# Kernel optimization log

Measured on AMD Instinct MI355X. Metric: run time of the kernel, lower is better.

Reference implementation:

```python
import jax, jax.numpy as jnp
import numpy as np

N_BAND = 5  # module hardcodes self.n = 5 -> keeps |i-j| <= N_BAND-1 = 4


def setup_inputs() -> dict:
    key = jax.random.key(0)
    ks = jax.random.split(key, 6)
    B, L, H = 4, 2048, 1024
    s = 1.0 / np.sqrt(H)
    return {
        "q": jax.random.normal(ks[0], (B, L, H), jnp.float32),
        "k": jax.random.normal(ks[1], (B, L, H), jnp.float32),
        "Wq": jax.random.normal(ks[2], (H, H), jnp.float32) * s,
        "bq": jax.random.normal(ks[3], (H,), jnp.float32) * s,
        "Wk": jax.random.normal(ks[4], (H, H), jnp.float32) * s,
        "bk": jax.random.normal(ks[5], (H,), jnp.float32) * s,
    }


def reference(q, k, Wq, bq, Wk, bk):
    b, l, e = q.shape
    # nn.Linear: y = x @ W^T + b
    qs = jnp.einsum("ble,he->blh", q, Wq) + bq
    ks = jnp.einsum("ble,he->blh", k, Wk) + bk
    # dense QK^T logits, [b, l, l]
    logits = jnp.einsum("blh,bmh->blm", qs, ks)
    # banded mask: the torch loop zeroes offsets 0..n-1 on both sides -> |i-j| <= n-1
    idx = jnp.arange(l)
    band = jnp.abs(idx[:, None] - idx[None, :]) <= (N_BAND - 1)  # [l, l]
    neg_inf = jnp.array(-jnp.inf, dtype=logits.dtype)
    logits = jnp.where(band[None, :, :], logits, neg_inf)
    # every row contains its diagonal, so softmax is well-defined
    return jax.nn.softmax(logits, axis=-1)
```

## Files before the change

kernel.cpp:

```cpp
#include <hip/hip_runtime.h>
#include <math.h>

#define LSEQ 2048
#define HDIM 1024
#define BATCH 4
#define ROWS (BATCH * LSEQ)
#define NBAND 9

typedef __attribute__((ext_vector_type(8))) short bf16x8;
typedef __attribute__((ext_vector_type(4))) float f32x4;
typedef __attribute__((ext_vector_type(8))) unsigned short u16x8;
typedef __attribute__((ext_vector_type(4))) unsigned uintx4;

#define AS3 __attribute__((address_space(3)))
#define AS1 __attribute__((address_space(1)))

__device__ __forceinline__ void gload16(const void* gp, void* lp) {
    __builtin_amdgcn_global_load_lds((AS1 const unsigned*)gp, (AS3 unsigned*)lp, 16, 0, 0);
}

__device__ __forceinline__ unsigned short f2bf(float x) {
    unsigned u = __float_as_uint(x);
    u += 0x7FFFu + ((u >> 16) & 1u);
    return (unsigned short)(u >> 16);
}
__device__ __forceinline__ float bf2f(unsigned short h) {
    return __uint_as_float(((unsigned)h) << 16);
}

__device__ __forceinline__ void split8(float4 a, float4 b, bf16x8& hi, bf16x8& lo) {
    float v[8] = {a.x, a.y, a.z, a.w, b.x, b.y, b.z, b.w};
#pragma unroll
    for (int j = 0; j < 8; j++) {
        unsigned short h = f2bf(v[j]);
        hi[j] = (short)h;
        lo[j] = (short)f2bf(v[j] - bf2f(h));
    }
}

__device__ __forceinline__ void unpack8(uintx4 w0, uintx4 w1, bf16x8& hi, bf16x8& lo) {
    union { bf16x8 v; uintx4 u; } H, L;
    H.u[0] = __builtin_amdgcn_perm(w0[1], w0[0], 0x05040100u);
    H.u[1] = __builtin_amdgcn_perm(w0[3], w0[2], 0x05040100u);
    H.u[2] = __builtin_amdgcn_perm(w1[1], w1[0], 0x05040100u);
    H.u[3] = __builtin_amdgcn_perm(w1[3], w1[2], 0x05040100u);
    L.u[0] = __builtin_amdgcn_perm(w0[1], w0[0], 0x07060302u);
    L.u[1] = __builtin_amdgcn_perm(w0[3], w0[2], 0x07060302u);
    L.u[2] = __builtin_amdgcn_perm(w1[1], w1[0], 0x07060302u);
    L.u[3] = __builtin_amdgcn_perm(w1[3], w1[2], 0x07060302u);
    hi = H.v; lo = L.v;
}

__global__ __launch_bounds__(256) void wpart_kernel(const float* __restrict__ Wk,
                                                    const float* __restrict__ bq,
                                                    float* __restrict__ wpart) {
    const int b = blockIdx.x;
    const int c0 = threadIdx.x * 4;
    float4 acc = {0.f, 0.f, 0.f, 0.f};
#pragma unroll
    for (int hh = 0; hh < 16; hh++) {
        const int h = b * 16 + hh;
        const float s = bq[h];
        float4 v = *reinterpret_cast<const float4*>(&Wk[(size_t)h * HDIM + c0]);
        acc.x += v.x * s; acc.y += v.y * s; acc.z += v.z * s; acc.w += v.w * s;
    }
    *reinterpret_cast<float4*>(&wpart[(size_t)b * HDIM + c0]) = acc;
}

__global__ __launch_bounds__(256) void wreduce(const float* __restrict__ wpart,
                                               float* __restrict__ w) {
    const int c = blockIdx.x * 256 + threadIdx.x;
    float s = 0.f;
#pragma unroll
    for (int b = 0; b < 64; b++) s += wpart[(size_t)b * HDIM + c];
    w[c] = s;
}

__global__ __launch_bounds__(256) void transpose_convert(const float* __restrict__ Wq,
                                                         const float* __restrict__ Wk,
                                                         unsigned short* __restrict__ qhi,
                                                         unsigned short* __restrict__ qlo,
                                                         unsigned short* __restrict__ khi,
                                                         unsigned short* __restrict__ klo) {
    __shared__ float tile[64][65];
    const int z = blockIdx.z;
    const float* src = z ? Wk : Wq;
    unsigned short* dh = z ? khi : qhi;
    unsigned short* dl = z ? klo : qlo;
    const int n0 = blockIdx.x * 64;
    const int h0 = blockIdx.y * 64;
    const int tid = threadIdx.x;

#pragma unroll
    for (int p = 0; p < 4; p++) {
        const int h = p * 16 + (tid >> 4);
        const int n = (tid & 15) * 4;
        float4 v = *reinterpret_cast<const float4*>(&src[(size_t)(h0 + h) * HDIM + n0 + n]);
        tile[h][n + 0] = v.x; tile[h][n + 1] = v.y; tile[h][n + 2] = v.z; tile[h][n + 3] = v.w;
    }
    __syncthreads();
#pragma unroll
    for (int p = 0; p < 2; p++) {
        const int n = p * 32 + (tid >> 3);
        const int h = (tid & 7) * 8;
        u16x8 hv, lv;
#pragma unroll
        for (int j = 0; j < 8; j++) {
            float x = tile[h + j][n];
            unsigned short hb = f2bf(x);
            hv[j] = hb;
            lv[j] = f2bf(x - bf2f(hb));
        }
        *reinterpret_cast<u16x8*>(&dh[(size_t)(n0 + n) * HDIM + h0 + h]) = hv;
        *reinterpret_cast<u16x8*>(&dl[(size_t)(n0 + n) * HDIM + h0 + h]) = lv;
    }
}

__global__ __launch_bounds__(256) void convert_k_beta(const float* __restrict__ k,
                                                      const float* __restrict__ w,
                                                      unsigned short* __restrict__ Xhi,
                                                      unsigned short* __restrict__ Xlo,
                                                      float* __restrict__ beta) {
    __shared__ float red[4];
    const int r = blockIdx.x;
    const int t = threadIdx.x;
    float4 v = *reinterpret_cast<const float4*>(&k[(size_t)r * HDIM + t * 4]);
    float4 wv = *reinterpret_cast<const float4*>(&w[t * 4]);
    ushort4 h, l;
    h.x = f2bf(v.x); l.x = f2bf(v.x - bf2f(h.x));
    h.y = f2bf(v.y); l.y = f2bf(v.y - bf2f(h.y));
    h.z = f2bf(v.z); l.z = f2bf(v.z - bf2f(h.z));
    h.w = f2bf(v.w); l.w = f2bf(v.w - bf2f(h.w));
    reinterpret_cast<ushort4*>(Xhi)[(size_t)r * 256 + t] = h;
    reinterpret_cast<ushort4*>(Xlo)[(size_t)r * 256 + t] = l;
    float d = v.x * wv.x + v.y * wv.y + v.z * wv.z + v.w * wv.w;
#pragma unroll
    for (int off = 32; off > 0; off >>= 1) d += __shfl_xor(d, off, 64);
    if ((t & 63) == 0) red[t >> 6] = d;
    __syncthreads();
    if (t == 0) beta[r] = red[0] + red[1] + red[2] + red[3];
}

__global__ __launch_bounds__(256, 2) void gemm_part(
        const unsigned short* __restrict__ Ahi, const unsigned short* __restrict__ Alo,
        const unsigned short* __restrict__ Bhi, const unsigned short* __restrict__ Blo,
        float* __restrict__ Cparts) {
    __shared__ unsigned short sh[4 * 4096];
    const int AHI = 0, ALO = 4096, BHI = 8192, BLO = 12288;
    const int tid = threadIdx.x;
    const int w = tid >> 6, l = tid & 63;
    const int wr = w >> 1, wc = w & 1;
    const int row0 = blockIdx.x * 128, col0 = blockIdx.y * 128;
    const int kbeg = blockIdx.z * 256;
    float* C = Cparts + (size_t)blockIdx.z * HDIM * HDIM;
    const int srow0 = (l >> 2), scbp = l & 3;

    f32x4 acc[4][4];
#pragma unroll
    for (int m = 0; m < 4; m++)
#pragma unroll
        for (int n = 0; n < 4; n++) acc[m][n] = (f32x4){0.f, 0.f, 0.f, 0.f};

    const int fr_a[4] = {wr * 64 + (l & 15), wr * 64 + 16 + (l & 15),
                         wr * 64 + 32 + (l & 15), wr * 64 + 48 + (l & 15)};
    const int fr_b[4] = {wc * 64 + (l & 15), wc * 64 + 16 + (l & 15),
                         wc * 64 + 32 + (l & 15), wc * 64 + 48 + (l & 15)};
    const int cb = l >> 4;

    for (int k0 = kbeg; k0 < kbeg + 256; k0 += 32) {
#pragma unroll
        for (int i = 0; i < 2; i++) {
            const int seg = i * 4 + w;
            const int row = seg * 16 + srow0;
            const int cbs = scbp ^ ((row >> 1) & 3);
            gload16(Ahi + (size_t)(row0 + row) * HDIM + k0 + cbs * 8, &sh[AHI + seg * 512]);
            gload16(Alo + (size_t)(row0 + row) * HDIM + k0 + cbs * 8, &sh[ALO + seg * 512]);
            gload16(Bhi + (size_t)(col0 + row) * HDIM + k0 + cbs * 8, &sh[BHI + seg * 512]);
            gload16(Blo + (size_t)(col0 + row) * HDIM + k0 + cbs * 8, &sh[BLO + seg * 512]);
        }
        __syncthreads();

        bf16x8 ah[4], al[4], bh[4], bl[4];
#pragma unroll
        for (int m = 0; m < 4; m++) {
            const int r = fr_a[m];
            const int cbs = cb ^ ((r >> 1) & 3);
            ah[m] = *reinterpret_cast<const bf16x8*>(&sh[AHI + r * 32 + cbs * 8]);
            al[m] = *reinterpret_cast<const bf16x8*>(&sh[ALO + r * 32 + cbs * 8]);
        }
#pragma unroll
        for (int n = 0; n < 4; n++) {
            const int r = fr_b[n];
            const int cbs = cb ^ ((r >> 1) & 3);
            bh[n] = *reinterpret_cast<const bf16x8*>(&sh[BHI + r * 32 + cbs * 8]);
            bl[n] = *reinterpret_cast<const bf16x8*>(&sh[BLO + r * 32 + cbs * 8]);
        }
#pragma unroll
        for (int m = 0; m < 4; m++)
#pragma unroll
            for (int n = 0; n < 4; n++) {
                acc[m][n] = __builtin_amdgcn_mfma_f32_16x16x32_bf16(ah[m], bh[n], acc[m][n], 0, 0, 0);
                acc[m][n] = __builtin_amdgcn_mfma_f32_16x16x32_bf16(ah[m], bl[n], acc[m][n], 0, 0, 0);
                acc[m][n] = __builtin_amdgcn_mfma_f32_16x16x32_bf16(al[m], bh[n], acc[m][n], 0, 0, 0);
            }
        __syncthreads();
    }

    const int lcol = l & 15, lrow = (l >> 4) * 4;
#pragma unroll
    for (int n = 0; n < 4; n++) {
        const int colg = col0 + wc * 64 + n * 16 + lcol;
#pragma unroll
        for (int m = 0; m < 4; m++) {
            const int rowg = row0 + wr * 64 + m * 16 + lrow;
#pragma unroll
            for (int v = 0; v < 4; v++)
                C[(size_t)(rowg + v) * HDIM + colg] = acc[m][n][v];
        }
    }
}

__global__ __launch_bounds__(256) void reduceM_convert(const float* __restrict__ Mparts,
                                                       unsigned short* __restrict__ Mhi,
                                                       unsigned short* __restrict__ Mlo) {
    const int idx4 = blockIdx.x * 256 + threadIdx.x;
    float4 s = {0.f, 0.f, 0.f, 0.f};
#pragma unroll
    for (int z = 0; z < 4; z++) {
        float4 v = reinterpret_cast<const float4*>(Mparts + (size_t)z * HDIM * HDIM)[idx4];
        s.x += v.x; s.y += v.y; s.z += v.z; s.w += v.w;
    }
    ushort4 h, l;
    h.x = f2bf(s.x); l.x = f2bf(s.x - bf2f(h.x));
    h.y = f2bf(s.y); l.y = f2bf(s.y - bf2f(h.y));
    h.z = f2bf(s.z); l.z = f2bf(s.z - bf2f(h.z));
    h.w = f2bf(s.w); l.w = f2bf(s.w - bf2f(h.w));
    reinterpret_cast<ushort4*>(Mhi)[idx4] = h;
    reinterpret_cast<ushort4*>(Mlo)[idx4] = l;
}

__global__ __launch_bounds__(256, 2) void gemm_t(
        const unsigned short* __restrict__ Ahi, const unsigned short* __restrict__ Alo,
        const unsigned short* __restrict__ Bhi, const unsigned short* __restrict__ Blo,
        unsigned* __restrict__ Tpack) {
    __shared__ unsigned short sh[2][16384];
    const int AHI = 0, ALO = 4096, BHI = 8192, BLO = 12288;
    const int tid = threadIdx.x;
    const int w = tid >> 6, l = tid & 63;
    const int wr = w >> 1, wc = w & 1;
    const int row0 = blockIdx.x * 128, col0 = blockIdx.y * 128;
    const int srow0 = (l >> 2), scbp = l & 3;

    f32x4 acc[4][4];
#pragma unroll
    for (int m = 0; m < 4; m++)
#pragma unroll
        for (int n = 0; n < 4; n++) acc[m][n] = (f32x4){0.f, 0.f, 0.f, 0.f};

    const int fr_a[4] = {wr * 64 + (l & 15), wr * 64 + 16 + (l & 15),
                         wr * 64 + 32 + (l & 15), wr * 64 + 48 + (l & 15)};
    const int fr_b[4] = {wc * 64 + (l & 15), wc * 64 + 16 + (l & 15),
                         wc * 64 + 32 + (l & 15), wc * 64 + 48 + (l & 15)};
    const int cb = l >> 4;

    auto stage = [&](int buf, int k0) {
#pragma unroll
        for (int i = 0; i < 2; i++) {
            const int seg = i * 4 + w;
            const int row = seg * 16 + srow0;
            const int cbs = scbp ^ ((row >> 1) & 3);
            gload16(Ahi + (size_t)(row0 + row) * HDIM + k0 + cbs * 8, &sh[buf][AHI + seg * 512]);
            gload16(Alo + (size_t)(row0 + row) * HDIM + k0 + cbs * 8, &sh[buf][ALO + seg * 512]);
            gload16(Bhi + (size_t)(col0 + row) * HDIM + k0 + cbs * 8, &sh[buf][BHI + seg * 512]);
            gload16(Blo + (size_t)(col0 + row) * HDIM + k0 + cbs * 8, &sh[buf][BLO + seg * 512]);
        }
    };
    auto compute = [&](int buf) {
        bf16x8 ah[4], al[4], bh[4], bl[4];
#pragma unroll
        for (int m = 0; m < 4; m++) {
            const int r = fr_a[m];
            const int cbs = cb ^ ((r >> 1) & 3);
            ah[m] = *reinterpret_cast<const bf16x8*>(&sh[buf][AHI + r * 32 + cbs * 8]);
            al[m] = *reinterpret_cast<const bf16x8*>(&sh[buf][ALO + r * 32 + cbs * 8]);
        }
#pragma unroll
        for (int n = 0; n < 4; n++) {
            const int r = fr_b[n];
            const int cbs = cb ^ ((r >> 1) & 3);
            bh[n] = *reinterpret_cast<const bf16x8*>(&sh[buf][BHI + r * 32 + cbs * 8]);
            bl[n] = *reinterpret_cast<const bf16x8*>(&sh[buf][BLO + r * 32 + cbs * 8]);
        }
#pragma unroll
        for (int m = 0; m < 4; m++)
#pragma unroll
            for (int n = 0; n < 4; n++) {
                acc[m][n] = __builtin_amdgcn_mfma_f32_16x16x32_bf16(ah[m], bh[n], acc[m][n], 0, 0, 0);
                acc[m][n] = __builtin_amdgcn_mfma_f32_16x16x32_bf16(ah[m], bl[n], acc[m][n], 0, 0, 0);
                acc[m][n] = __builtin_amdgcn_mfma_f32_16x16x32_bf16(al[m], bh[n], acc[m][n], 0, 0, 0);
            }
    };

    stage(0, 0);
    __syncthreads();
    int cur = 0;
    for (int t = 0; t < 31; t++) {
        stage(cur ^ 1, (t + 1) * 32);
        compute(cur);
        __syncthreads();
        cur ^= 1;
    }
    compute(cur);

    const int lcol = l & 15, lrow = (l >> 4) * 4;
#pragma unroll
    for (int n = 0; n < 4; n++) {
        const int colg = col0 + wc * 64 + n * 16 + lcol;
#pragma unroll
        for (int m = 0; m < 4; m++) {
            const int rowg = row0 + wr * 64 + m * 16 + lrow;
#pragma unroll
            for (int v = 0; v < 4; v++) {
                const float x = acc[m][n][v];
                const unsigned short h = f2bf(x);
                const unsigned short lo = f2bf(x - bf2f(h));
                Tpack[(size_t)(rowg + v) * HDIM + colg] = (unsigned)h | ((unsigned)lo << 16);
            }
        }
    }
}

__global__ __launch_bounds__(256) void band_mfma(const float* __restrict__ q,
                                                 const unsigned* __restrict__ tpack,
                                                 const float* __restrict__ beta,
                                                 float* __restrict__ band) {
    __shared__ float lds_c[4][16][33];
    const int tid = threadIdx.x;
    const int w = tid >> 6, l = tid & 63;
    const int r0 = blockIdx.x * 16;
    const int b = r0 >> 11;
    const int i0 = r0 & (LSEQ - 1);
    const int fr = l & 15;
    const int kb = (l >> 4) * 8;

    const float* qrow = q + (size_t)(r0 + fr) * HDIM;
    const size_t tb = (size_t)b * LSEQ * HDIM;

    const int j0 = i0 - 4 + fr;
    const int j1 = i0 + 12 + fr;
    const int j0c = min(max(j0, 0), LSEQ - 1);
    const int j1c = min(max(j1, 0), LSEQ - 1);
    const bool v0 = (j0 >= 0) && (j0 < LSEQ);
    const bool v1 = (j1 >= 0) && (j1 < LSEQ);
    const bool interior = (i0 >= 4) && (i0 + 19 < LSEQ);
    const uintx4 uz = {0u, 0u, 0u, 0u};

    f32x4 c0 = {0.f, 0.f, 0.f, 0.f};
    f32x4 c1 = {0.f, 0.f, 0.f, 0.f};

#pragma unroll 2
    for (int ks = 0; ks < 8; ks++) {
        const int k0 = w * 256 + ks * 32 + kb;
        float4 qa = *reinterpret_cast<const float4*>(qrow + k0);
        float4 qb = *reinterpret_cast<const float4*>(qrow + k0 + 4);
        uintx4 w00 = *reinterpret_cast<const uintx4*>(&tpack[tb + (size_t)j0c * HDIM + k0]);
        uintx4 w01 = *reinterpret_cast<const uintx4*>(&tpack[tb + (size_t)j0c * HDIM + k0 + 4]);
        uintx4 w10 = *reinterpret_cast<const uintx4*>(&tpack[tb + (size_t)j1c * HDIM + k0]);
        uintx4 w11 = *reinterpret_cast<const uintx4*>(&tpack[tb + (size_t)j1c * HDIM + k0 + 4]);
        if (!interior) {
            if (!v0) { w00 = uz; w01 = uz; }
            if (!v1) { w10 = uz; w11 = uz; }
        }
        bf16x8 ah, al, b0h, b0l, b1h, b1l;
        split8(qa, qb, ah, al);
        unpack8(w00, w01, b0h, b0l);
        unpack8(w10, w11, b1h, b1l);
        c0 = __builtin_amdgcn_mfma_f32_16x16x32_bf16(ah, b0h, c0, 0, 0, 0);
        c0 = __builtin_amdgcn_mfma_f32_16x16x32_bf16(ah, b0l, c0, 0, 0, 0);
        c0 = __builtin_amdgcn_mfma_f32_16x16x32_bf16(al, b0h, c0, 0, 0, 0);
        c1 = __builtin_amdgcn_mfma_f32_16x16x32_bf16(ah, b1h, c1, 0, 0, 0);
        c1 = __builtin_amdgcn_mfma_f32_16x16x32_bf16(ah, b1l, c1, 0, 0, 0);
        c1 = __builtin_amdgcn_mfma_f32_16x16x32_bf16(al, b1h, c1, 0, 0, 0);
    }

#pragma unroll
    for (int v = 0; v < 4; v++) {
        lds_c[w][(l >> 4) * 4 + v][fr] = c0[v];
        lds_c[w][(l >> 4) * 4 + v][16 + fr] = c1[v];
    }
    __syncthreads();

#pragma unroll
    for (int e = tid; e < 512; e += 256) {
        const int rr = e >> 5, cc = e & 31;
        lds_c[0][rr][cc] = lds_c[0][rr][cc] + lds_c[1][rr][cc] +
                           lds_c[2][rr][cc] + lds_c[3][rr][cc];
    }
    __syncthreads();

    if (tid < 16) {
        const int il = i0 + tid;
        const int ig = r0 + tid;
        float lg[NBAND];
#pragma unroll
        for (int d = 0; d < NBAND; d++) {
            const int j = il + d - 4;
            lg[d] = (j >= 0 && j < LSEQ)
                    ? lds_c[0][tid][tid + d] + beta[(size_t)b * LSEQ + j]
                    : -1e30f;
        }
        float m = -1e30f;
#pragma unroll
        for (int d = 0; d < NBAND; d++) m = fmaxf(m, lg[d]);
        float p[NBAND], s = 0.f;
#pragma unroll
        for (int d = 0; d < NBAND; d++) { p[d] = expf(lg[d] - m); s += p[d]; }
        const float inv = 1.f / s;
#pragma unroll
        for (int d = 0; d < NBAND; d++) band[(size_t)ig * NBAND + d] = p[d] * inv;
    }
}

__global__ __launch_bounds__(256) void expand_band(const float* __restrict__ band,
                                                   float* __restrict__ out) {
    const size_t idx4 = (size_t)blockIdx.x * 256 + threadIdx.x;
    const size_t flat = idx4 * 4;
    const int j0 = (int)(flat & (LSEQ - 1));
    const size_t row = flat >> 11;
    const int i = (int)(row & (LSEQ - 1));
    float v[4];
#pragma unroll
    for (int s = 0; s < 4; s++) {
        const int dj = (j0 + s) - i + 4;
        v[s] = (dj >= 0 && dj < NBAND) ? band[row * NBAND + dj] : 0.f;
    }
    float4 o = {v[0], v[1], v[2], v[3]};
    *reinterpret_cast<float4*>(&out[flat]) = o;
}

__global__ __launch_bounds__(256) void gemm_nt_bias(const float* __restrict__ A,
                                                    const float* __restrict__ B,
                                                    const float* __restrict__ bias,
                                                    float* __restrict__ C) {
    __shared__ float As[8][132];
    __shared__ float Bs[8][132];
    const int tid = threadIdx.x;
    const int row0 = blockIdx.x * 128, col0 = blockIdx.y * 128;
    const int lr = tid >> 1, lc = (tid & 1) * 4;
    const int tx = tid & 15, ty = tid >> 4;
    float acc[2][2][4][4];
#pragma unroll
    for (int a = 0; a < 2; a++)
#pragma unroll
        for (int b = 0; b < 2; b++)
#pragma unroll
            for (int c = 0; c < 4; c++)
#pragma unroll
                for (int d = 0; d < 4; d++) acc[a][b][c][d] = 0.f;
    for (int k0 = 0; k0 < HDIM; k0 += 8) {
        float4 av = *reinterpret_cast<const float4*>(&A[(size_t)(row0 + lr) * HDIM + k0 + lc]);
        float4 bv = *reinterpret_cast<const float4*>(&B[(size_t)(col0 + lr) * HDIM + k0 + lc]);
        __syncthreads();
        As[lc + 0][lr] = av.x; As[lc + 1][lr] = av.y; As[lc + 2][lr] = av.z; As[lc + 3][lr] = av.w;
        Bs[lc + 0][lr] = bv.x; Bs[lc + 1][lr] = bv.y; Bs[lc + 2][lr] = bv.z; Bs[lc + 3][lr] = bv.w;
        __syncthreads();
#pragma unroll
        for (int kk = 0; kk < 8; kk++) {
            float4 a0 = *reinterpret_cast<const float4*>(&As[kk][ty * 4]);
            float4 a1 = *reinterpret_cast<const float4*>(&As[kk][64 + ty * 4]);
            float4 b0 = *reinterpret_cast<const float4*>(&Bs[kk][tx * 4]);
            float4 b1 = *reinterpret_cast<const float4*>(&Bs[kk][64 + tx * 4]);
            float am[2][4] = {{a0.x, a0.y, a0.z, a0.w}, {a1.x, a1.y, a1.z, a1.w}};
            float bw[2][4] = {{b0.x, b0.y, b0.z, b0.w}, {b1.x, b1.y, b1.z, b1.w}};
#pragma unroll
            for (int mi = 0; mi < 2; mi++)
#pragma unroll
                for (int ni = 0; ni < 2; ni++)
#pragma unroll
                    for (int mm = 0; mm < 4; mm++)
#pragma unroll
                        for (int nn = 0; nn < 4; nn++)
                            acc[mi][ni][mm][nn] += am[mi][mm] * bw[ni][nn];
        }
    }
#pragma unroll
    for (int mi = 0; mi < 2; mi++)
#pragma unroll
        for (int mm = 0; mm < 4; mm++) {
            const int r = row0 + mi * 64 + ty * 4 + mm;
#pragma unroll
            for (int ni = 0; ni < 2; ni++) {
                const int c = col0 + ni * 64 + tx * 4;
                float4 o;
                o.x = acc[mi][ni][mm][0] + bias[c + 0];
                o.y = acc[mi][ni][mm][1] + bias[c + 1];
                o.z = acc[mi][ni][mm][2] + bias[c + 2];
                o.w = acc[mi][ni][mm][3] + bias[c + 3];
                *reinterpret_cast<float4*>(&C[(size_t)r * HDIM + c]) = o;
            }
        }
}

__global__ __launch_bounds__(256) void band_softmax(const float* __restrict__ qs,
                                                    const float* __restrict__ ks,
                                                    float* __restrict__ band) {
    const int wave = threadIdx.x >> 6;
    const int lane = threadIdx.x & 63;
    const int r = blockIdx.x * 4 + wave;
    const int b = r >> 11;
    const int i = r & (LSEQ - 1);
    const float* qrow = qs + (size_t)r * HDIM;
    const float* kbase = ks + (size_t)b * LSEQ * HDIM;
    float acc[NBAND];
#pragma unroll
    for (int d = 0; d < NBAND; d++) acc[d] = 0.f;
    for (int h = lane; h < HDIM; h += 64) {
        const float qv = qrow[h];
#pragma unroll
        for (int d = 0; d < NBAND; d++) {
            const int j = i + d - 4;
            if (j >= 0 && j < LSEQ)
                acc[d] += qv * kbase[(size_t)j * HDIM + h];
        }
    }
#pragma unroll
    for (int d = 0; d < NBAND; d++) {
        float v = acc[d];
#pragma unroll
        for (int off = 32; off > 0; off >>= 1) v += __shfl_xor(v, off, 64);
        acc[d] = v;
    }
    if (lane == 0) {
        float m = -1e30f;
#pragma unroll
        for (int d = 0; d < NBAND; d++) {
            const int j = i + d - 4;
            if (j >= 0 && j < LSEQ) m = fmaxf(m, acc[d]);
        }
        float p[NBAND];
        float s = 0.f;
#pragma unroll
        for (int d = 0; d < NBAND; d++) {
            const int j = i + d - 4;
            p[d] = (j >= 0 && j < LSEQ) ? expf(acc[d] - m) : 0.f;
            s += p[d];
        }
        const float inv = 1.f / s;
#pragma unroll
        for (int d = 0; d < NBAND; d++) band[(size_t)r * NBAND + d] = p[d] * inv;
    }
}

extern "C" void kernel_launch(void* const* d_in, const int* in_sizes, int n_in,
                              void* d_out, int out_size, void* d_ws, size_t ws_size,
                              hipStream_t stream) {
    const float* q  = (const float*)d_in[0];
    const float* k  = (const float*)d_in[1];
    const float* Wq = (const float*)d_in[2];
    const float* bq = (const float*)d_in[3];
    const float* Wk = (const float*)d_in[4];
    const float* bk = (const float*)d_in[5];
    float* out = (float*)d_out;

    const size_t bandB = (size_t)ROWS * NBAND * sizeof(float);
    char* p = (char*)d_ws;
    float* band = (float*)p;                 p += bandB;
    unsigned short* Xhi = (unsigned short*)p; p += (size_t)ROWS * HDIM * 2;
    unsigned short* Xlo = (unsigned short*)p; p += (size_t)ROWS * HDIM * 2;
    unsigned short* Mhi = (unsigned short*)p; p += (size_t)HDIM * HDIM * 2;
    unsigned short* Mlo = (unsigned short*)p; p += (size_t)HDIM * HDIM * 2;
    float* w        = (float*)p;             p += HDIM * sizeof(float);
    float* wpart    = (float*)p;             p += 64 * HDIM * sizeof(float);
    float* beta     = (float*)p;             p += ROWS * sizeof(float);
    const size_t need = (size_t)(p - (char*)d_ws);

    unsigned short* WqTh = Xhi;
    unsigned short* WqTl = Xhi + (size_t)HDIM * HDIM;
    unsigned short* WkTh = Xhi + 2 * (size_t)HDIM * HDIM;
    unsigned short* WkTl = Xhi + 3 * (size_t)HDIM * HDIM;

    unsigned* tpack = (unsigned*)out;
    float* Mparts = (float*)((char*)out + 32ull * 1024 * 1024);

    if (ws_size >= need) {
        wpart_kernel<<<64, 256, 0, stream>>>(Wk, bq, wpart);
        wreduce<<<4, 256, 0, stream>>>(wpart, w);
        dim3 tg(16, 16, 2);
        transpose_convert<<<tg, 256, 0, stream>>>(Wq, Wk, WqTh, WqTl, WkTh, WkTl);
        dim3 mg(8, 8, 4);
        gemm_part<<<mg, 256, 0, stream>>>(WqTh, WqTl, WkTh, WkTl, Mparts);
        reduceM_convert<<<HDIM * HDIM / 4 / 256, 256, 0, stream>>>(Mparts, Mhi, Mlo);
        convert_k_beta<<<ROWS, 256, 0, stream>>>(k, w, Xhi, Xlo, beta);
        dim3 gg(ROWS / 128, HDIM / 128);
        gemm_t<<<gg, 256, 0, stream>>>(Xhi, Xlo, Mhi, Mlo, tpack);
        band_mfma<<<ROWS / 16, 256, 0, stream>>>(q, tpack, beta, band);
        expand_band<<<(size_t)ROWS * LSEQ / 4 / 256, 256, 0, stream>>>(band, out);
    } else {
        float* qs = out;
        float* ks = out + (size_t)ROWS * HDIM;
        dim3 gg(ROWS / 128, HDIM / 128);
        gemm_nt_bias<<<gg, 256, 0, stream>>>(q, Wq, bq, qs);
        gemm_nt_bias<<<gg, 256, 0, stream>>>(k, Wk, bk, ks);
        band_softmax<<<ROWS / 4, 256, 0, stream>>>(qs, ks, band);
        expand_band<<<(size_t)ROWS * LSEQ / 4 / 256, 256, 0, stream>>>(band, out);
    }
}
```

Baseline: 140.6 us.

## Fuse small prep kernels and enlarge gemm_t tile to 256 rows with 512 threads

After: 133.1 us. -5.3%, faster.

```diff
diff --git a/kernel.cpp b/kernel.cpp
--- a/kernel.cpp
+++ b/kernel.cpp
@@ -51,45 +51,37 @@
     hi = H.v; lo = L.v;
 }
 
-__global__ __launch_bounds__(256) void wpart_kernel(const float* __restrict__ Wk,
-                                                    const float* __restrict__ bq,
-                                                    float* __restrict__ wpart) {
-    const int b = blockIdx.x;
-    const int c0 = threadIdx.x * 4;
-    float4 acc = {0.f, 0.f, 0.f, 0.f};
-#pragma unroll
-    for (int hh = 0; hh < 16; hh++) {
-        const int h = b * 16 + hh;
-        const float s = bq[h];
-        float4 v = *reinterpret_cast<const float4*>(&Wk[(size_t)h * HDIM + c0]);
-        acc.x += v.x * s; acc.y += v.y * s; acc.z += v.z * s; acc.w += v.w * s;
-    }
-    *reinterpret_cast<float4*>(&wpart[(size_t)b * HDIM + c0]) = acc;
-}
-
-__global__ __launch_bounds__(256) void wreduce(const float* __restrict__ wpart,
-                                               float* __restrict__ w) {
-    const int c = blockIdx.x * 256 + threadIdx.x;
-    float s = 0.f;
-#pragma unroll
-    for (int b = 0; b < 64; b++) s += wpart[(size_t)b * HDIM + c];
-    w[c] = s;
-}
-
-__global__ __launch_bounds__(256) void transpose_convert(const float* __restrict__ Wq,
-                                                         const float* __restrict__ Wk,
-                                                         unsigned short* __restrict__ qhi,
-                                                         unsigned short* __restrict__ qlo,
-                                                         unsigned short* __restrict__ khi,
-                                                         unsigned short* __restrict__ klo) {
+__global__ __launch_bounds__(256) void tcw_kernel(const float* __restrict__ Wq,
+                                                  const float* __restrict__ Wk,
+                                                  const float* __restrict__ bq,
+                                                  unsigned short* __restrict__ qhi,
+                                                  unsigned short* __restrict__ qlo,
+                                                  unsigned short* __restrict__ khi,
+                                                  unsigned short* __restrict__ klo,
+                                                  float* __restrict__ wpart) {
+    const int z = blockIdx.z;
+    const int tid = threadIdx.x;
+    if (z == 2) {
+        const int fid = blockIdx.y * 16 + blockIdx.x;
+        if (fid >= 64) return;
+        const int c0 = tid * 4;
+        float4 acc = {0.f, 0.f, 0.f, 0.f};
+#pragma unroll
+        for (int hh = 0; hh < 16; hh++) {
+            const int h = fid * 16 + hh;
+            const float s = bq[h];
+            float4 v = *reinterpret_cast<const float4*>(&Wk[(size_t)h * HDIM + c0]);
+            acc.x += v.x * s; acc.y += v.y * s; acc.z += v.z * s; acc.w += v.w * s;
+        }
+        *reinterpret_cast<float4*>(&wpart[(size_t)fid * HDIM + c0]) = acc;
+        return;
+    }
     __shared__ float tile[64][65];
-    const int z = blockIdx.z;
     const float* src = z ? Wk : Wq;
     unsigned short* dh = z ? khi : qhi;
     unsigned short* dl = z ? klo : qlo;
     const int n0 = blockIdx.x * 64;
     const int h0 = blockIdx.y * 64;
-    const int tid = threadIdx.x;
 
 #pragma unroll
     for (int p = 0; p < 4; p++) {
@@ -220,9 +212,19 @@
     }
 }
 
-__global__ __launch_bounds__(256) void reduceM_convert(const float* __restrict__ Mparts,
-                                                       unsigned short* __restrict__ Mhi,
-                                                       unsigned short* __restrict__ Mlo) {
+__global__ __launch_bounds__(256) void reduceMw_convert(const float* __restrict__ Mparts,
+                                                        unsigned short* __restrict__ Mhi,
+                                                        unsigned short* __restrict__ Mlo,
+                                                        const float* __restrict__ wpart,
+                                                        float* __restrict__ w) {
+    if (blockIdx.x >= 1024) {
+        const int c = (blockIdx.x - 1024) * 256 + threadIdx.x;
+        float s = 0.f;
+#pragma unroll
+        for (int b = 0; b < 64; b++) s += wpart[(size_t)b * HDIM + c];
+        w[c] = s;
+        return;
+    }
     const int idx4 = blockIdx.x * 256 + threadIdx.x;
     float4 s = {0.f, 0.f, 0.f, 0.f};
 #pragma unroll
@@ -239,16 +241,16 @@
     reinterpret_cast<ushort4*>(Mlo)[idx4] = l;
 }
 
-__global__ __launch_bounds__(256, 2) void gemm_t(
+__global__ __launch_bounds__(512, 2) void gemm_t(
         const unsigned short* __restrict__ Ahi, const unsigned short* __restrict__ Alo,
         const unsigned short* __restrict__ Bhi, const unsigned short* __restrict__ Blo,
         unsigned* __restrict__ Tpack) {
-    __shared__ unsigned short sh[2][16384];
-    const int AHI = 0, ALO = 4096, BHI = 8192, BLO = 12288;
+    __shared__ unsigned short sh[2][24576];
+    const int AHI = 0, ALO = 8192, BHI = 16384, BLO = 20480;
     const int tid = threadIdx.x;
     const int w = tid >> 6, l = tid & 63;
     const int wr = w >> 1, wc = w & 1;
-    const int row0 = blockIdx.x * 128, col0 = blockIdx.y * 128;
+    const int row0 = blockIdx.x * 256, col0 = blockIdx.y * 128;
     const int srow0 = (l >> 2), scbp = l & 3;
 
     f32x4 acc[4][4];
@@ -266,11 +268,16 @@
     auto stage = [&](int buf, int k0) {
 #pragma unroll
         for (int i = 0; i < 2; i++) {
-            const int seg = i * 4 + w;
+            const int seg = i * 8 + w;
             const int row = seg * 16 + srow0;
             const int cbs = scbp ^ ((row >> 1) & 3);
             gload16(Ahi + (size_t)(row0 + row) * HDIM + k0 + cbs * 8, &sh[buf][AHI + seg * 512]);
             gload16(Alo + (size_t)(row0 + row) * HDIM + k0 + cbs * 8, &sh[buf][ALO + seg * 512]);
+        }
+        {
+            const int seg = w;
+            const int row = seg * 16 + srow0;
+            const int cbs = scbp ^ ((row >> 1) & 3);
             gload16(Bhi + (size_t)(col0 + row) * HDIM + k0 + cbs * 8, &sh[buf][BHI + seg * 512]);
             gload16(Blo + (size_t)(col0 + row) * HDIM + k0 + cbs * 8, &sh[buf][BLO + seg * 512]);
         }
@@ -583,16 +590,14 @@
     float* Mparts = (float*)((char*)out + 32ull * 1024 * 1024);
 
     if (ws_size >= need) {
-        wpart_kernel<<<64, 256, 0, stream>>>(Wk, bq, wpart);
-        wreduce<<<4, 256, 0, stream>>>(wpart, w);
-        dim3 tg(16, 16, 2);
-        transpose_convert<<<tg, 256, 0, stream>>>(Wq, Wk, WqTh, WqTl, WkTh, WkTl);
+        dim3 tg(16, 16, 3);
+        tcw_kernel<<<tg, 256, 0, stream>>>(Wq, Wk, bq, WqTh, WqTl, WkTh, WkTl, wpart);
         dim3 mg(8, 8, 4);
         gemm_part<<<mg, 256, 0, stream>>>(WqTh, WqTl, WkTh, WkTl, Mparts);
-        reduceM_convert<<<HDIM * HDIM / 4 / 256, 256, 0, stream>>>(Mparts, Mhi, Mlo);
+        reduceMw_convert<<<1028, 256, 0, stream>>>(Mparts, Mhi, Mlo, wpart, w);
         convert_k_beta<<<ROWS, 256, 0, stream>>>(k, w, Xhi, Xlo, beta);
-        dim3 gg(ROWS / 128, HDIM / 128);
-        gemm_t<<<gg, 256, 0, stream>>>(Xhi, Xlo, Mhi, Mlo, tpack);
+        dim3 gg(ROWS / 256, HDIM / 128);
+        gemm_t<<<gg, 512, 0, stream>>>(Xhi, Xlo, Mhi, Mlo, tpack);
         band_mfma<<<ROWS / 16, 256, 0, stream>>>(q, tpack, beta, band);
         expand_band<<<(size_t)ROWS * LSEQ / 4 / 256, 256, 0, stream>>>(band, out);
     } else {
```
